# Performance work log

Measured on AMD Instinct MI355X. Metric: run time of the kernel, lower is better.

The kernel has to match this reference:

```python
import jax, jax.numpy as jnp
import numpy as np

D_MODEL = 96
D_INNER = 192        # expand_factor * d_model
D_STATE = 16
DT_RANK = 6          # ceil(d_model / 16)
D_CONV = 4
N_LAYERS = 2
EPS = 1e-5


def conv3d(x, w, b=None, padding=((0, 0), (0, 0), (0, 0)), groups=1):
    # x: (N, C, L, H, W), w: (O, C//groups, kL, kH, kW)
    y = jax.lax.conv_general_dilated(
        x, w, window_strides=(1, 1, 1), padding=padding,
        dimension_numbers=('NCDHW', 'OIDHW', 'NCDHW'),
        feature_group_count=groups)
    return y if b is None else y + b[None, :, None, None, None]


def rmsnorm(x, w):
    # faithful to source: mean of squares over the LAST dim (W)
    return x * jax.lax.rsqrt(jnp.mean(x * x, axis=-1, keepdims=True) + EPS) * w


def mamba_block(x, p):
    # x: (N, d_model, L, H, W)
    L = x.shape[2]
    xz = conv3d(x, p['in_proj_w'], padding=((0, 0), (1, 1), (1, 1)))
    xi, z = xz[:, :D_INNER], xz[:, D_INNER:]
    # causal depthwise temporal conv: pad d_conv-1, crop to L
    xi = conv3d(xi, p['conv1d_w'], p['conv1d_b'],
                padding=((D_CONV - 1, D_CONV - 1), (0, 0), (0, 0)),
                groups=D_INNER)[:, :, :L]
    xi = jax.nn.silu(xi)
    # --- SSM (selective scan, pscan path) ---
    A = -jnp.exp(p['A_log'])                                   # (K, S)
    dbc = conv3d(xi, p['x_proj_w'])                            # (N, dt_rank+2S, L, H, W)
    delta = jax.nn.softplus(conv3d(dbc[:, :DT_RANK], p['dt_proj_w'], p['dt_proj_b']))  # (N, K, L, H, W)
    B = jnp.moveaxis(dbc[:, DT_RANK:DT_RANK + D_STATE], 1, -1)  # (N, L, H, W, S)
    C = dbc[:, DT_RANK + D_STATE:]                              # (N, S, L, H, W)
    deltaA = jnp.exp(delta[..., None] * A[None, :, None, None, None, :])  # (N,K,L,H,W,S)
    BX = delta[..., None] * B[:, None] * xi[..., None]                    # (N,K,L,H,W,S)

    def op(e1, e2):
        a1, b1 = e1
        a2, b2 = e2
        return a1 * a2, a2 * b1 + b2

    _, hs = jax.lax.associative_scan(op, (deltaA, BX), axis=2)  # scan over L
    y = jnp.einsum('nklhws,nslhw->nklhw', hs, C) + p['D'][None, :, None, None, None] * xi
    out = y * jax.nn.silu(z)
    return conv3d(out, p['out_proj_w'])


def _forward(x, in_proj_w, conv1d_w, conv1d_b, x_proj_w, dt_proj_w,
             dt_proj_b, A_log, D, out_proj_w, norm_w):
    for l in range(N_LAYERS):
        p = dict(in_proj_w=in_proj_w[l], conv1d_w=conv1d_w[l], conv1d_b=conv1d_b[l],
                 x_proj_w=x_proj_w[l], dt_proj_w=dt_proj_w[l], dt_proj_b=dt_proj_b[l],
                 A_log=A_log[l], D=D[l], out_proj_w=out_proj_w[l], norm_w=norm_w[l])
        x = mamba_block(rmsnorm(x, p['norm_w']), p) + x   # ResidualBlock
        x = x[:, :, 0:1]                                   # Mamba.forward keeps t=0 only
    return x


def setup_inputs() -> dict:
    key = jax.random.key(0)
    ks = jax.random.split(key, 12)
    Lk = N_LAYERS
    x = jax.random.normal(ks[0], (2, D_MODEL, 8, 24, 24), dtype=jnp.float32)
    in_proj_w = jax.random.normal(ks[1], (Lk, 2 * D_INNER, D_MODEL, 1, 3, 3), jnp.float32) * (D_MODEL * 9) ** -0.5
    conv1d_w = jax.random.normal(ks[2], (Lk, D_INNER, 1, D_CONV, 1, 1), jnp.float32) * D_CONV ** -0.5
    conv1d_b = jax.random.normal(ks[3], (Lk, D_INNER), jnp.float32) * 0.02
    x_proj_w = jax.random.normal(ks[4], (Lk, DT_RANK + 2 * D_STATE, D_INNER, 1, 1, 1), jnp.float32) * D_INNER ** -0.5
    dt_std = DT_RANK ** -0.5
    dt_proj_w = jax.random.uniform(ks[5], (Lk, D_INNER, DT_RANK, 1, 1, 1), jnp.float32, -dt_std, dt_std)
    # dt bias init: inv softplus of dt ~ LogUniform(dt_min, dt_max)
    dt = jnp.exp(jax.random.uniform(ks[6], (Lk, D_INNER), jnp.float32)
                 * (np.log(0.1) - np.log(0.001)) + np.log(0.001))
    dt = jnp.clip(dt, 1e-4, None)
    dt_proj_b = dt + jnp.log(-jnp.expm1(-dt))
    A_log = jnp.log(jnp.tile(jnp.arange(1, D_STATE + 1, dtype=jnp.float32), (Lk, D_INNER, 1)))
    D = jnp.ones((Lk, D_INNER), jnp.float32)
    out_proj_w = jax.random.normal(ks[7], (Lk, D_MODEL, D_INNER, 1, 1, 1), jnp.float32) * D_INNER ** -0.5
    norm_w = jnp.ones((Lk, 1, D_MODEL, 1, 1, 1), jnp.float32)
    return {'x': x, 'in_proj_w': in_proj_w, 'conv1d_w': conv1d_w, 'conv1d_b': conv1d_b,
            'x_proj_w': x_proj_w, 'dt_proj_w': dt_proj_w, 'dt_proj_b': dt_proj_b,
            'A_log': A_log, 'D': D, 'out_proj_w': out_proj_w, 'norm_w': norm_w}


def reference(x, in_proj_w, conv1d_w, conv1d_b, x_proj_w, dt_proj_w,
              dt_proj_b, A_log, D, out_proj_w, norm_w):
    return _forward(x, in_proj_w, conv1d_w, conv1d_b, x_proj_w, dt_proj_w,
                    dt_proj_b, A_log, D, out_proj_w, norm_w)
```

## Files before the change

### kernel.cpp

```cpp
#include <hip/hip_runtime.h>
#include <math.h>

#define NB   2
#define CM   96
#define CI   192
#define CO   384
#define HP   24
#define WP   24
#define PX   576
#define DTR  6
#define NDBC 38
#define CSPLIT 2
#define CCH  48

__device__ __forceinline__ float siluf(float x){ return x / (1.f + expf(-x)); }
__device__ __forceinline__ float softplusf(float x){ return x > 20.f ? x : log1pf(expf(x)); }
__device__ __forceinline__ unsigned short f2bf(float f){
    unsigned u = __float_as_uint(f);
    return (unsigned short)((u + 0x7fffu + ((u >> 16) & 1u)) >> 16);
}
__device__ __forceinline__ float bflo(unsigned u){ return __uint_as_float(u << 16); }
__device__ __forceinline__ float bfhi(unsigned u){ return __uint_as_float(u & 0xffff0000u); }

#define NW_IN (2*CO*CM*9)
#define WQB_L (CM*CO*8)
#define WRB_L (CM*CO)
#define WPT_L (CI*CM)
__global__ void prep_k(const float* __restrict__ ipw, const float* __restrict__ opw,
                       unsigned short* __restrict__ wQb, unsigned short* __restrict__ wRb,
                       float* __restrict__ wpT){
    int idx = blockIdx.x*256 + threadIdx.x;
    if (idx < NW_IN){
        int l = idx / (CO*CM*9);
        int r = idx % (CO*CM*9);
        int o = r / (CM*9);
        int r2 = r % (CM*9);
        int c = r2 / 9;
        int k = r2 % 9;
        unsigned short v = f2bf(ipw[idx]);
        if (k < 8) wQb[(long)l*WQB_L + ((c*CO + o)<<3) + k] = v;
        else       wRb[(long)l*WRB_L + c*CO + o] = v;
    } else {
        int j = idx - NW_IN;
        if (j < 2*CI*CM){
            int l = j / (CI*CM);
            int r = j % (CI*CM);
            int c = r / CM;
            int m = r % CM;
            wpT[l*WPT_L + c*CM + m] = opw[(l*CM + m)*CI + c];
        }
    }
}

__global__ __launch_bounds__(256) void conv_k(
    const float* __restrict__ x, long nStr, long cStr,
    const float* __restrict__ nw,
    const unsigned short* __restrict__ wQb, const unsigned short* __restrict__ wRb,
    float* __restrict__ acc)
{
    __shared__ float hs[CCH][3][28];
    __shared__ float scl[CCH][3];
    int bx = blockIdx.x;
    int og = blockIdx.y;
    int cs = blockIdx.z;
    int n  = bx / HP, hh = bx % HP;
    int tid = threadIdx.x;
    int c0 = cs*CCH;

    if (tid < CCH*3){
        int c = tid/3, j = tid%3;
        int row = hh + j - 1;
        float s = 0.f;
        if (row >= 0 && row < HP){
            const float4* xp4 = (const float4*)(x + (long)n*nStr + (long)(c0+c)*cStr + row*WP);
            #pragma unroll
            for (int w4 = 0; w4 < WP/4; w4++){
                float4 v = xp4[w4];
                s += v.x*v.x + v.y*v.y + v.z*v.z + v.w*v.w;
            }
            s = rsqrtf(s*(1.0f/WP) + 1e-5f) * nw[c0+c];
        }
        scl[c][j] = s;
    }
    __syncthreads();

    for (int idx = tid; idx < CCH*3*28; idx += 256){
        int c = idx/84; int rem = idx%84; int j = rem/28; int wc = rem%28;
        int row = hh + j - 1;
        float v = 0.f;
        if (row >= 0 && row < HP && wc >= 1 && wc <= WP)
            v = x[(long)n*nStr + (long)(c0+c)*cStr + row*WP + (wc-1)] * scl[c][j];
        hs[c][j][wc] = v;
    }
    __syncthreads();

    int ol = tid & 63;
    int o  = og*64 + ol;
    int x0 = (tid >> 6) * 6;
    float a0[6] = {0,0,0,0,0,0};
    const uint4* wq4 = (const uint4*)wQb;

    for (int c = 0; c < CCH; c++){
        int cg = c0 + c;
        uint4 wv = wq4[cg*CO + o];
        float w0 = bflo(wv.x), w1 = bfhi(wv.x);
        float w2 = bflo(wv.y), w3 = bfhi(wv.y);
        float w4 = bflo(wv.z), w5 = bfhi(wv.z);
        float w6 = bflo(wv.w), w7 = bfhi(wv.w);
        float w8 = bflo((unsigned)wRb[cg*CO + o]);
        float r0v[8], r1v[8], r2v[8];
        #pragma unroll
        for (int i = 0; i < 4; i++){
            float2 p0 = *(const float2*)(&hs[c][0][x0] + 2*i);
            float2 p1 = *(const float2*)(&hs[c][1][x0] + 2*i);
            float2 p2 = *(const float2*)(&hs[c][2][x0] + 2*i);
            r0v[2*i] = p0.x; r0v[2*i+1] = p0.y;
            r1v[2*i] = p1.x; r1v[2*i+1] = p1.y;
            r2v[2*i] = p2.x; r2v[2*i+1] = p2.y;
        }
        #pragma unroll
        for (int p = 0; p < 6; p++){
            a0[p] += w0*r0v[p] + w1*r0v[p+1] + w2*r0v[p+2]
                   + w3*r1v[p] + w4*r1v[p+1] + w5*r1v[p+2]
                   + w6*r2v[p] + w7*r2v[p+1] + w8*r2v[p+2];
        }
    }

    float* ap = acc + ((long)(cs*NB + n)*PX + hh*WP + x0)*CO + o;
    #pragma unroll
    for (int p = 0; p < 6; p++) ap[p*CO] = a0[p];
}

__global__ __launch_bounds__(256) void ssm_k(
    const float* __restrict__ acc,
    const float* __restrict__ c1w, const float* __restrict__ c1b,
    const float* __restrict__ xpw, const float* __restrict__ dtw,
    const float* __restrict__ dtb, const float* __restrict__ Dp,
    const float* __restrict__ wpT,
    const float* __restrict__ xres, long nStrR, long cStrR,
    float* __restrict__ dst)
{
    __shared__ float gl[4][CI];
    int wave = threadIdx.x >> 6, lane = threadIdx.x & 63;
    int p  = blockIdx.x*4 + wave;
    int n  = p / PX, px = p % PX;
    float* glw = gl[wave];

    float xi[3], sz[3];
    #pragma unroll
    for (int t = 0; t < 3; t++){
        int c = lane + 64*t;
        float xr = 0.f, zr = 0.f;
        #pragma unroll
        for (int q = 0; q < CSPLIT; q++){
            const float* ap = acc + ((long)(q*NB + n)*PX + px)*CO;
            xr += ap[c]; zr += ap[CI + c];
        }
        xi[t] = siluf(xr*c1w[c*4 + 3] + c1b[c]);
        sz[t] = siluf(zr);
    }

    float dbc[NDBC];
    #pragma unroll
    for (int j = 0; j < NDBC; j++){
        float s = 0.f;
        #pragma unroll
        for (int t = 0; t < 3; t++) s += xi[t]*xpw[j*CI + lane + 64*t];
        dbc[j] = s;
    }
    #pragma unroll
    for (int step = 1; step < 64; step <<= 1){
        #pragma unroll
        for (int j = 0; j < NDBC; j++) dbc[j] += __shfl_xor(dbc[j], step, 64);
    }
    float BC = 0.f;
    #pragma unroll
    for (int si = 0; si < 16; si++) BC += dbc[6+si]*dbc[22+si];

    #pragma unroll
    for (int t = 0; t < 3; t++){
        int c = lane + 64*t;
        float dl = dtb[c];
        #pragma unroll
        for (int r = 0; r < DTR; r++) dl += dbc[r]*dtw[c*DTR + r];
        dl = softplusf(dl);
        glw[c] = xi[t]*(dl*BC + Dp[c])*sz[t];
    }
    asm volatile("s_waitcnt lgkmcnt(0)" ::: "memory");

    #pragma unroll
    for (int mi = 0; mi < 2; mi++){
        int m = mi*64 + lane;
        if (m < CM){
            float s0 = 0.f, s1 = 0.f, s2 = 0.f, s3 = 0.f;
            for (int c = 0; c < CI; c += 4){
                const float4 g4 = *(const float4*)(glw + c);
                s0 += g4.x*wpT[(c+0)*CM + m];
                s1 += g4.y*wpT[(c+1)*CM + m];
                s2 += g4.z*wpT[(c+2)*CM + m];
                s3 += g4.w*wpT[(c+3)*CM + m];
            }
            float s = (s0+s1) + (s2+s3);
            s += xres[(long)n*nStrR + (long)m*cStrR + px];
            dst[(n*CM + m)*PX + px] = s;
        }
    }
}

extern "C" void kernel_launch(void* const* d_in, const int* in_sizes, int n_in,
                              void* d_out, int out_size, void* d_ws, size_t ws_size,
                              hipStream_t stream) {
    const float* x_in = (const float*)d_in[0];
    const float* ipw  = (const float*)d_in[1];
    const float* c1w  = (const float*)d_in[2];
    const float* c1b  = (const float*)d_in[3];
    const float* xpw  = (const float*)d_in[4];
    const float* dtw  = (const float*)d_in[5];
    const float* dtb  = (const float*)d_in[6];
    const float* Dp   = (const float*)d_in[8];
    const float* opw  = (const float*)d_in[9];
    const float* nw   = (const float*)d_in[10];

    char* ws = (char*)d_ws;
    unsigned short* wQb = (unsigned short*)ws;
    unsigned short* wRb = wQb + 2*WQB_L;
    float* wpT = (float*)(wRb + 2*WRB_L);
    float* acc = wpT + 2*WPT_L;
    float* x1  = acc + (long)CSPLIT*NB*PX*CO;

    prep_k<<<(NW_IN + 2*CI*CM + 255)/256, 256, 0, stream>>>(ipw, opw, wQb, wRb, wpT);

    conv_k<<<dim3(NB*HP, 6, CSPLIT), 256, 0, stream>>>(
        x_in, 96L*8*PX, 8L*PX, nw, wQb, wRb, acc);
    ssm_k<<<NB*PX/4, 256, 0, stream>>>(
        acc, c1w, c1b, xpw, dtw, dtb, Dp, wpT,
        x_in, 96L*8*PX, 8L*PX, x1);

    conv_k<<<dim3(NB*HP, 6, CSPLIT), 256, 0, stream>>>(
        x1, 96L*PX, (long)PX, nw + CM, wQb + WQB_L, wRb + WRB_L, acc);
    ssm_k<<<NB*PX/4, 256, 0, stream>>>(
        acc, c1w + CI*4, c1b + CI, xpw + NDBC*CI, dtw + CI*DTR, dtb + CI, Dp + CI, wpT + WPT_L,
        x1, 96L*PX, (long)PX, (float*)d_out);
}
```

Baseline: 172.9 us.

## Drop weight prep kernel, read fp32 weights directly, split conv channels eightfold

Removes the prep kernel that converted in_proj weights to bf16 in a transposed layout and transposed out_proj weights. Each layer now reads the original fp32 weights directly: conv reads 9 contiguous taps per (o,c) and ssm reads out_proj rows as float4. The conv channel split goes from 2 to 8 chunks of 12 channels, so the grid has more blocks and the ssm kernel sums more partial accumulators. This saves a launch and the conversion pass, but the conv weight loads become strided across lanes (uncoalesced) and the accumulator traffic grows.

Result: slower. 200.2 us (+15.8%).

```diff
diff --git a/kernel.cpp b/kernel.cpp
--- a/kernel.cpp
+++ b/kernel.cpp
@@ -10,52 +10,17 @@
 #define PX   576
 #define DTR  6
 #define NDBC 38
-#define CSPLIT 2
-#define CCH  48
+#define CSPLIT 8
+#define CCH  12
+#define IPW_L (CO*CM*9)
 
 __device__ __forceinline__ float siluf(float x){ return x / (1.f + expf(-x)); }
 __device__ __forceinline__ float softplusf(float x){ return x > 20.f ? x : log1pf(expf(x)); }
-__device__ __forceinline__ unsigned short f2bf(float f){
-    unsigned u = __float_as_uint(f);
-    return (unsigned short)((u + 0x7fffu + ((u >> 16) & 1u)) >> 16);
-}
-__device__ __forceinline__ float bflo(unsigned u){ return __uint_as_float(u << 16); }
-__device__ __forceinline__ float bfhi(unsigned u){ return __uint_as_float(u & 0xffff0000u); }
-
-#define NW_IN (2*CO*CM*9)
-#define WQB_L (CM*CO*8)
-#define WRB_L (CM*CO)
-#define WPT_L (CI*CM)
-__global__ void prep_k(const float* __restrict__ ipw, const float* __restrict__ opw,
-                       unsigned short* __restrict__ wQb, unsigned short* __restrict__ wRb,
-                       float* __restrict__ wpT){
-    int idx = blockIdx.x*256 + threadIdx.x;
-    if (idx < NW_IN){
-        int l = idx / (CO*CM*9);
-        int r = idx % (CO*CM*9);
-        int o = r / (CM*9);
-        int r2 = r % (CM*9);
-        int c = r2 / 9;
-        int k = r2 % 9;
-        unsigned short v = f2bf(ipw[idx]);
-        if (k < 8) wQb[(long)l*WQB_L + ((c*CO + o)<<3) + k] = v;
-        else       wRb[(long)l*WRB_L + c*CO + o] = v;
-    } else {
-        int j = idx - NW_IN;
-        if (j < 2*CI*CM){
-            int l = j / (CI*CM);
-            int r = j % (CI*CM);
-            int c = r / CM;
-            int m = r % CM;
-            wpT[l*WPT_L + c*CM + m] = opw[(l*CM + m)*CI + c];
-        }
-    }
-}
 
 __global__ __launch_bounds__(256) void conv_k(
     const float* __restrict__ x, long nStr, long cStr,
     const float* __restrict__ nw,
-    const unsigned short* __restrict__ wQb, const unsigned short* __restrict__ wRb,
+    const float* __restrict__ ipw,
     float* __restrict__ acc)
 {
     __shared__ float hs[CCH][3][28];
@@ -98,16 +63,13 @@
     int o  = og*64 + ol;
     int x0 = (tid >> 6) * 6;
     float a0[6] = {0,0,0,0,0,0};
-    const uint4* wq4 = (const uint4*)wQb;
 
     for (int c = 0; c < CCH; c++){
         int cg = c0 + c;
-        uint4 wv = wq4[cg*CO + o];
-        float w0 = bflo(wv.x), w1 = bfhi(wv.x);
-        float w2 = bflo(wv.y), w3 = bfhi(wv.y);
-        float w4 = bflo(wv.z), w5 = bfhi(wv.z);
-        float w6 = bflo(wv.w), w7 = bfhi(wv.w);
-        float w8 = bflo((unsigned)wRb[cg*CO + o]);
+        const float* wp = ipw + (long)o*(CM*9) + cg*9;
+        float w0 = wp[0], w1 = wp[1], w2 = wp[2];
+        float w3 = wp[3], w4 = wp[4], w5 = wp[5];
+        float w6 = wp[6], w7 = wp[7], w8 = wp[8];
         float r0v[8], r1v[8], r2v[8];
         #pragma unroll
         for (int i = 0; i < 4; i++){
@@ -136,7 +98,7 @@
     const float* __restrict__ c1w, const float* __restrict__ c1b,
     const float* __restrict__ xpw, const float* __restrict__ dtw,
     const float* __restrict__ dtb, const float* __restrict__ Dp,
-    const float* __restrict__ wpT,
+    const float* __restrict__ opw,
     const float* __restrict__ xres, long nStrR, long cStrR,
     float* __restrict__ dst)
 {
@@ -192,13 +154,15 @@
     for (int mi = 0; mi < 2; mi++){
         int m = mi*64 + lane;
         if (m < CM){
+            const float* wr = opw + (long)m*CI;
             float s0 = 0.f, s1 = 0.f, s2 = 0.f, s3 = 0.f;
             for (int c = 0; c < CI; c += 4){
                 const float4 g4 = *(const float4*)(glw + c);
-                s0 += g4.x*wpT[(c+0)*CM + m];
-                s1 += g4.y*wpT[(c+1)*CM + m];
-                s2 += g4.z*wpT[(c+2)*CM + m];
-                s3 += g4.w*wpT[(c+3)*CM + m];
+                const float4 w4 = *(const float4*)(wr + c);
+                s0 += g4.x*w4.x;
+                s1 += g4.y*w4.y;
+                s2 += g4.z*w4.z;
+                s3 += g4.w*w4.w;
             }
             float s = (s0+s1) + (s2+s3);
             s += xres[(long)n*nStrR + (long)m*cStrR + px];
@@ -222,23 +186,19 @@
     const float* nw   = (const float*)d_in[10];
 
     char* ws = (char*)d_ws;
-    unsigned short* wQb = (unsigned short*)ws;
-    unsigned short* wRb = wQb + 2*WQB_L;
-    float* wpT = (float*)(wRb + 2*WRB_L);
-    float* acc = wpT + 2*WPT_L;
+    float* acc = (float*)ws;
     float* x1  = acc + (long)CSPLIT*NB*PX*CO;
 
-    prep_k<<<(NW_IN + 2*CI*CM + 255)/256, 256, 0, stream>>>(ipw, opw, wQb, wRb, wpT);
-
     conv_k<<<dim3(NB*HP, 6, CSPLIT), 256, 0, stream>>>(
-        x_in, 96L*8*PX, 8L*PX, nw, wQb, wRb, acc);
+        x_in, 96L*8*PX, 8L*PX, nw, ipw, acc);
     ssm_k<<<NB*PX/4, 256, 0, stream>>>(
-        acc, c1w, c1b, xpw, dtw, dtb, Dp, wpT,
+        acc, c1w, c1b, xpw, dtw, dtb, Dp, opw,
         x_in, 96L*8*PX, 8L*PX, x1);
 
     conv_k<<<dim3(NB*HP, 6, CSPLIT), 256, 0, stream>>>(
-        x1, 96L*PX, (long)PX, nw + CM, wQb + WQB_L, wRb + WRB_L, acc);
+        x1, 96L*PX, (long)PX, nw + CM, ipw + IPW_L, acc);
     ssm_k<<<NB*PX/4, 256, 0, stream>>>(
-        acc, c1w + CI*4, c1b + CI, xpw + NDBC*CI, dtw + CI*DTR, dtb + CI, Dp + CI, wpT + WPT_L,
+        acc, c1w + CI*4, c1b + CI, xpw + NDBC*CI, dtw + CI*DTR, dtb + CI, Dp + CI,
+        opw + CM*CI,
         x1, 96L*PX, (long)PX, (float*)d_out);
 }
```
